# Optimization experiments

Measured on AMD Instinct MI355X. Metric: run time of the kernel, lower is better.

Reference implementation:

```python
import jax, jax.numpy as jnp
import numpy as np

HIDDEN = 1024
NUM_HEADS = 16
HEAD_DIM = HIDDEN // NUM_HEADS  # 64


def setup_inputs() -> dict:
    key = jax.random.key(0)
    ks = jax.random.split(key, 10)
    B, S = 2, 2048
    X = jax.random.normal(ks[0], (B, S, HIDDEN), dtype=jnp.float32)
    attention_mask = jnp.ones((B, 1, 1, S), dtype=jnp.int32)
    s = 1.0 / np.sqrt(HIDDEN)
    Wq = jax.random.uniform(ks[1], (HIDDEN, NUM_HEADS * HEAD_DIM), jnp.float32, -s, s)
    bq = jnp.zeros((NUM_HEADS * HEAD_DIM,), jnp.float32)
    Wk = jax.random.uniform(ks[2], (HIDDEN, HEAD_DIM), jnp.float32, -s, s)
    bk = jnp.zeros((HEAD_DIM,), jnp.float32)
    Wv = jax.random.uniform(ks[3], (HIDDEN, HEAD_DIM), jnp.float32, -s, s)
    bv = jnp.zeros((HEAD_DIM,), jnp.float32)
    Wo = jax.random.uniform(ks[4], (HIDDEN, HIDDEN), jnp.float32, -s, s)
    bo = jnp.zeros((HIDDEN,), jnp.float32)
    return {"X": X, "Wq": Wq, "bq": bq, "Wk": Wk, "bk": bk,
            "Wv": Wv, "bv": bv, "Wo": Wo, "bo": bo,
            "attention_mask": attention_mask}


def reference(X, Wq, bq, Wk, bk, Wv, bv, Wo, bo, attention_mask):
    B, S, _ = X.shape
    H, D = NUM_HEADS, HEAD_DIM
    # projections
    q = (X @ Wq + bq).reshape(B, S, H, D).transpose(0, 2, 1, 3)  # [B,H,S,D]
    k = (X @ Wk + bk)  # [B,S,D] single KV head
    v = (X @ Wv + bv)  # [B,S,D]
    # scores: broadcast single KV head across all query heads (repeat_interleave equiv)
    scores = jnp.einsum("bhsd,btd->bhst", q, k) / np.sqrt(D)  # [B,H,S,S]
    scores = jnp.where(attention_mask == 0, -jnp.inf, scores)
    weights = jax.nn.softmax(scores, axis=-1)
    # dropout in eval mode -> identity
    out = jnp.einsum("bhst,btd->bhsd", weights, v)  # [B,H,S,D]
    out = out.transpose(0, 2, 1, 3).reshape(B, S, H * D)
    return out @ Wo + bo
```

## Files before the change

### kernel.cpp

```cpp
#include <hip/hip_runtime.h>
#include <hip/hip_bf16.h>
#include <stdint.h>


#define DI __device__ __forceinline__

typedef unsigned short u16;
typedef __attribute__((ext_vector_type(8))) __bf16 bf16x8;
typedef __attribute__((ext_vector_type(4))) float f32x4;
typedef __attribute__((ext_vector_type(4))) float float4v;
typedef __attribute__((ext_vector_type(4))) u16 u16x4;

DI u16 f2bf(float f) {
  union { float f; unsigned int u; } v; v.f = f;
  unsigned int u = v.u;
  return (u16)((u + 0x7FFFu + ((u >> 16) & 1u)) >> 16);
}

DI void async16(void* lds, const void* g) {
  __builtin_amdgcn_global_load_lds(
      (const __attribute__((address_space(1))) unsigned int*)g,
      (__attribute__((address_space(3))) unsigned int*)lds, 16, 0, 0);
}

DI void stage_rows(const u16* __restrict__ g, long gstride, char* lds,
                   int nchunks, int tid) {
  int w = tid >> 6, lane = tid & 63;
  for (int base = w * 64; base < nchunks; base += 256) {
    int chunk = base + lane;
    int row = chunk >> 3;
    int cc = (chunk & 7) ^ (row & 7);
    async16(lds + base * 16, g + (long)row * gstride + cc * 8);
  }
}

DI bf16x8 read_frag(const char* lds, int row, int kchunk) {
  return *(const bf16x8*)(lds + row * 128 + ((kchunk ^ (row & 7)) << 4));
}

DI f32x4 MFMA(bf16x8 a, bf16x8 b, f32x4 c) {
  return __builtin_amdgcn_mfma_f32_16x16x32_bf16(a, b, c, 0, 0, 0);
}


__global__ void cvt_f32_bf16_kernel(const float* __restrict__ src,
                                    u16* __restrict__ dst, int n4) {
  int i = blockIdx.x * blockDim.x + threadIdx.x;
  if (i >= n4) return;
  float4v v = *(const float4v*)(src + (long)i * 4);
  u16x4 o;
  o[0] = f2bf(v[0]); o[1] = f2bf(v[1]); o[2] = f2bf(v[2]); o[3] = f2bf(v[3]);
  *(u16x4*)(dst + (long)i * 4) = o;
}

__global__ void transpose_f32_bf16(const float* __restrict__ src,
                                   u16* __restrict__ dst, int K, int N) {
  __shared__ float t[32][33];
  int nt = blockIdx.x % (N >> 5), kt = blockIdx.x / (N >> 5);
  int c = threadIdx.x & 31, r0 = threadIdx.x >> 5;
#pragma unroll
  for (int i = 0; i < 4; i++) {
    int r = r0 + i * 8;
    t[r][c] = src[(long)(kt * 32 + r) * N + nt * 32 + c];
  }
  __syncthreads();
#pragma unroll
  for (int i = 0; i < 4; i++) {
    int r = r0 + i * 8;
    dst[(long)(nt * 32 + r) * K + kt * 32 + c] = f2bf(t[c][r]);
  }
}


template <int EPI, int BN>
__global__ __launch_bounds__(256, 3) void gemm_bf16(
    const u16* __restrict__ A, const u16* __restrict__ Bt, int N, int K,
    u16* __restrict__ Qb, u16* __restrict__ Kb, u16* __restrict__ Vt,
    const float* __restrict__ bq, const float* __restrict__ bk,
    const float* __restrict__ bv, float* __restrict__ Cout,
    const float* __restrict__ bo) {
  constexpr int NF = BN / 32;
  constexpr int ACH = 1024, BCH = BN * 8;
  __shared__ __attribute__((aligned(16))) char lds[2][16384 + BN * 128];
  const int tid = threadIdx.x, lane = tid & 63, w = tid >> 6;
  const int nTiles = N / BN;
  const int mt = blockIdx.x / nTiles, nt = blockIdx.x % nTiles;
  const int m0 = mt << 7, n0 = nt * BN;
  const int wm = w >> 1, wn = w & 1;
  const int lrow = lane & 15, lk = lane >> 4;

  f32x4 acc[4][NF] = {};

  stage_rows(A + (long)m0 * K, K, lds[0], ACH, tid);
  stage_rows(Bt + (long)n0 * K, K, lds[0] + 16384, BCH, tid);
  __syncthreads();

  const int NT = K >> 6;
  int cur = 0;
  for (int t = 0; t < NT; t++) {
    if (t + 1 < NT) {
      stage_rows(A + (long)m0 * K + (t + 1) * 64, K, lds[cur ^ 1], ACH, tid);
      stage_rows(Bt + (long)n0 * K + (t + 1) * 64, K, lds[cur ^ 1] + 16384,
                 BCH, tid);
    }
    const char* La = lds[cur];
    const char* Lb = lds[cur] + 16384;
#pragma unroll
    for (int kk = 0; kk < 2; kk++) {
      bf16x8 af[4], bfr[NF];
#pragma unroll
      for (int i = 0; i < 4; i++)
        af[i] = read_frag(La, wm * 64 + i * 16 + lrow, kk * 4 + lk);
#pragma unroll
      for (int i = 0; i < NF; i++)
        bfr[i] = read_frag(Lb, wn * (BN / 2) + i * 16 + lrow, kk * 4 + lk);
#pragma unroll
      for (int mf = 0; mf < 4; mf++)
#pragma unroll
        for (int nf = 0; nf < NF; nf++)
          acc[mf][nf] = MFMA(af[mf], bfr[nf], acc[mf][nf]);
    }
    __syncthreads();
    cur ^= 1;
  }

#pragma unroll
  for (int mf = 0; mf < 4; mf++) {
#pragma unroll
    for (int nf = 0; nf < NF; nf++) {
      int col = n0 + wn * (BN / 2) + nf * 16 + lrow;
#pragma unroll
      for (int r = 0; r < 4; r++) {
        int row = m0 + wm * 64 + mf * 16 + lk * 4 + r;
        float x = acc[mf][nf][r];
        if (EPI == 0) {
          if (col < 1024) {
            Qb[(long)row * 1024 + col] = f2bf((x + bq[col]) * 0.125f);
          } else if (col < 1088) {
            int d = col - 1024;
            Kb[(long)row * 64 + d] = f2bf(x + bk[d]);
          } else {
            int d = col - 1088;
            int b = row >> 11, s = row & 2047;
            Vt[((long)(b * 64 + d)) * 2048 + s] = f2bf(x + bv[d]);
          }
        } else {
          Cout[(long)row * 1024 + col] = x + bo[col];
        }
      }
    }
  }
}

__global__ __launch_bounds__(256, 4) void attn_kernel(
    const u16* __restrict__ Qb, const u16* __restrict__ Kb,
    const u16* __restrict__ Vt, u16* __restrict__ attnb) {
  __shared__ __attribute__((aligned(16))) char ldsQP[8192];
  __shared__ __attribute__((aligned(16))) char ldsK[2][8192];
  __shared__ __attribute__((aligned(16))) char ldsV[2][8192];

  const int tid = threadIdx.x, lane = tid & 63, w = tid >> 6;
  const int lrow = lane & 15, lk = lane >> 4;
  const int qt = blockIdx.x & 31;
  const int bh = blockIdx.x >> 5;
  const int b = bh >> 4, h = bh & 15;
  const int q0 = qt << 6;

  const u16* Qg = Qb + ((long)(b * 2048 + q0)) * 1024 + h * 64;
  const u16* Kg = Kb + ((long)b * 2048) * 64;
  const u16* Vg = Vt + ((long)b * 64) * 2048;

  stage_rows(Qg, 1024, ldsQP, 512, tid);
  stage_rows(Kg, 64, ldsK[0], 512, tid);
  stage_rows(Vg, 2048, ldsV[0], 512, tid);
  __syncthreads();

  bf16x8 qa[2];
#pragma unroll
  for (int kk = 0; kk < 2; kk++)
    qa[kk] = read_frag(ldsQP, w * 16 + lrow, kk * 4 + lk);

  f32x4 acc[4] = {};
  float m_run[4], l_run[4];
#pragma unroll
  for (int r = 0; r < 4; r++) { m_run[r] = -1e30f; l_run[r] = 0.f; }

  bf16x8 vones;
#pragma unroll
  for (int i = 0; i < 8; i++) vones[i] = (__bf16)1.0f;

  int cur = 0;
  for (int t = 0; t < 32; t++) {
    if (t + 1 < 32) {
      stage_rows(Kg + (t + 1) * 64 * 64, 64, ldsK[cur ^ 1], 512, tid);
      stage_rows(Vg + (t + 1) * 64, 2048, ldsV[cur ^ 1], 512, tid);
    }
    f32x4 s[4] = {};
    __builtin_amdgcn_s_setprio(1);
#pragma unroll
    for (int kk = 0; kk < 2; kk++) {
      bf16x8 kb[4];
#pragma unroll
      for (int kf = 0; kf < 4; kf++)
        kb[kf] = read_frag(ldsK[cur], kf * 16 + lrow, kk * 4 + lk);
#pragma unroll
      for (int kf = 0; kf < 4; kf++)
        s[kf] = MFMA(qa[kk], kb[kf], s[kf]);
    }
    __builtin_amdgcn_s_setprio(0);
#pragma unroll
    for (int r = 0; r < 4; r++) {
      float mx = fmaxf(fmaxf(s[0][r], s[1][r]), fmaxf(s[2][r], s[3][r]));
#pragma unroll
      for (int msk = 1; msk < 16; msk <<= 1)
        mx = fmaxf(mx, __shfl_xor(mx, msk));
      if (mx > m_run[r] + 8.f) {
        float alpha = __expf(m_run[r] - mx);
        m_run[r] = mx;
        l_run[r] *= alpha;
#pragma unroll
        for (int df = 0; df < 4; df++) acc[df][r] *= alpha;
      }
      int q = w * 16 + lk * 4 + r;
      char* prow = ldsQP + q * 128;
      int sw = (q & 7) << 4;
#pragma unroll
      for (int kf = 0; kf < 4; kf++) {
        float p = __expf(s[kf][r] - m_run[r]);
        int col = kf * 16 + lrow;
        *(u16*)(prow + (((col >> 3) << 4) ^ sw) + (col & 7) * 2) = f2bf(p);
      }
    }
    f32x4 lsum = {};
    __builtin_amdgcn_s_setprio(1);
#pragma unroll
    for (int kk = 0; kk < 2; kk++) {
      bf16x8 pa = read_frag(ldsQP, w * 16 + lrow, kk * 4 + lk);
      bf16x8 vb[4];
#pragma unroll
      for (int df = 0; df < 4; df++)
        vb[df] = read_frag(ldsV[cur], df * 16 + lrow, kk * 4 + lk);
#pragma unroll
      for (int df = 0; df < 4; df++)
        acc[df] = MFMA(pa, vb[df], acc[df]);
      lsum = MFMA(pa, vones, lsum);
    }
    __builtin_amdgcn_s_setprio(0);
#pragma unroll
    for (int r = 0; r < 4; r++) l_run[r] += lsum[r];
    __syncthreads();
    cur ^= 1;
  }

#pragma unroll
  for (int df = 0; df < 4; df++)
#pragma unroll
    for (int r = 0; r < 4; r++) {
      int qrow = q0 + w * 16 + lk * 4 + r;
      int col = h * 64 + df * 16 + lrow;
      float o = acc[df][r] / l_run[r];
      attnb[((long)(b * 2048 + qrow)) * 1024 + col] = f2bf(o);
    }
}


extern "C" void kernel_launch(void* const* d_in, const int* in_sizes, int n_in,
                              void* d_out, int out_size, void* d_ws,
                              size_t ws_size, hipStream_t stream) {
  const float* X  = (const float*)d_in[0];
  const float* Wq = (const float*)d_in[1];
  const float* bq = (const float*)d_in[2];
  const float* Wk = (const float*)d_in[3];
  const float* bk = (const float*)d_in[4];
  const float* Wv = (const float*)d_in[5];
  const float* bv = (const float*)d_in[6];
  const float* Wo = (const float*)d_in[7];
  const float* bo = (const float*)d_in[8];
  float* out = (float*)d_out;

  char* ws = (char*)d_ws;
  u16* Xbf   = (u16*)(ws);
  u16* WqkvT = (u16*)(ws + 8388608);
  u16* WoT   = (u16*)(ws + 10747904);
  u16* Qb    = (u16*)(ws + 12845056);
  u16* Kb    = (u16*)(ws + 21233664);
  u16* Vt    = (u16*)(ws + 21757952);
  u16* attnb = (u16*)(ws + 22282240);

  cvt_f32_bf16_kernel<<<4096, 256, 0, stream>>>(X, Xbf, 1048576);
  transpose_f32_bf16<<<1024, 256, 0, stream>>>(Wq, WqkvT, 1024, 1024);
  transpose_f32_bf16<<<64, 256, 0, stream>>>(Wk, WqkvT + 1024 * 1024, 1024, 64);
  transpose_f32_bf16<<<64, 256, 0, stream>>>(Wv, WqkvT + 1088 * 1024, 1024, 64);
  transpose_f32_bf16<<<1024, 256, 0, stream>>>(Wo, WoT, 1024, 1024);

  gemm_bf16<0, 64><<<576, 256, 0, stream>>>(Xbf, WqkvT, 1152, 1024, Qb, Kb, Vt,
                                            bq, bk, bv, nullptr, nullptr);
  attn_kernel<<<1024, 256, 0, stream>>>(Qb, Kb, Vt, attnb);
  gemm_bf16<1, 64><<<512, 256, 0, stream>>>(attnb, WoT, 1024, 1024, nullptr,
                                            nullptr, nullptr, nullptr, nullptr,
                                            nullptr, out, bo);
}
```

Before: 223.6 us.

## Rewrite attention with 32x32 MFMA, register-resident P, and exp2 softmax

The attention kernel now computes transposed scores S^T = K·Q^T with 32x32x16 MFMAs, so each lane holds one query column and the row max needs only one cross-lane shuffle. The probabilities are packed into bf16 and exchanged between lane halves with shuffles, which removes the LDS round-trip for P. The query tile grows to 128 rows per block (512 blocks, occupancy hint lowered to 2), and K/V staging is folded into one double-buffered LDS array. Q is pre-scaled by log2(e)/8 so exp2f can replace __expf. The price is more registers per lane and half as many blocks.

```diff
diff --git a/kernel.cpp b/kernel.cpp
--- a/kernel.cpp
+++ b/kernel.cpp
@@ -6,15 +6,23 @@
 #define DI __device__ __forceinline__
 
 typedef unsigned short u16;
+typedef unsigned int u32;
 typedef __attribute__((ext_vector_type(8))) __bf16 bf16x8;
 typedef __attribute__((ext_vector_type(4))) float f32x4;
+typedef __attribute__((ext_vector_type(16))) float f32x16;
 typedef __attribute__((ext_vector_type(4))) float float4v;
 typedef __attribute__((ext_vector_type(4))) u16 u16x4;
+typedef __attribute__((ext_vector_type(4))) u32 u32x4;
+typedef __attribute__((ext_vector_type(2))) u32 u32x2;
 
 DI u16 f2bf(float f) {
   union { float f; unsigned int u; } v; v.f = f;
   unsigned int u = v.u;
   return (u16)((u + 0x7FFFu + ((u >> 16) & 1u)) >> 16);
+}
+
+DI u32 pk2(float lo, float hi) {
+  return (u32)f2bf(lo) | ((u32)f2bf(hi) << 16);
 }
 
 DI void async16(void* lds, const void* g) {
@@ -40,6 +48,9 @@
 
 DI f32x4 MFMA(bf16x8 a, bf16x8 b, f32x4 c) {
   return __builtin_amdgcn_mfma_f32_16x16x32_bf16(a, b, c, 0, 0, 0);
+}
+DI f32x16 MFMA32(bf16x8 a, bf16x8 b, f32x16 c) {
+  return __builtin_amdgcn_mfma_f32_32x32x16_bf16(a, b, c, 0, 0, 0);
 }
 
 
@@ -135,7 +146,7 @@
         float x = acc[mf][nf][r];
         if (EPI == 0) {
           if (col < 1024) {
-            Qb[(long)row * 1024 + col] = f2bf((x + bq[col]) * 0.125f);
+            Qb[(long)row * 1024 + col] = f2bf((x + bq[col]) * 0.18033688f);
           } else if (col < 1088) {
             int d = col - 1024;
             Kb[(long)row * 64 + d] = f2bf(x + bk[d]);
@@ -152,114 +163,122 @@
   }
 }
 
-__global__ __launch_bounds__(256, 4) void attn_kernel(
+__global__ __launch_bounds__(256, 2) void attn_kernel(
     const u16* __restrict__ Qb, const u16* __restrict__ Kb,
     const u16* __restrict__ Vt, u16* __restrict__ attnb) {
-  __shared__ __attribute__((aligned(16))) char ldsQP[8192];
-  __shared__ __attribute__((aligned(16))) char ldsK[2][8192];
-  __shared__ __attribute__((aligned(16))) char ldsV[2][8192];
+  __shared__ __attribute__((aligned(16))) char ldsKV[2][16384];
 
   const int tid = threadIdx.x, lane = tid & 63, w = tid >> 6;
-  const int lrow = lane & 15, lk = lane >> 4;
-  const int qt = blockIdx.x & 31;
-  const int bh = blockIdx.x >> 5;
+  const int cq = lane & 31, hi = lane >> 5;
+  const int qt = blockIdx.x & 15;
+  const int bh = blockIdx.x >> 4;
   const int b = bh >> 4, h = bh & 15;
-  const int q0 = qt << 6;
+  const int q0 = qt << 7;
 
   const u16* Qg = Qb + ((long)(b * 2048 + q0)) * 1024 + h * 64;
   const u16* Kg = Kb + ((long)b * 2048) * 64;
   const u16* Vg = Vt + ((long)b * 64) * 2048;
 
-  stage_rows(Qg, 1024, ldsQP, 512, tid);
-  stage_rows(Kg, 64, ldsK[0], 512, tid);
-  stage_rows(Vg, 2048, ldsV[0], 512, tid);
-  __syncthreads();
-
-  bf16x8 qa[2];
-#pragma unroll
-  for (int kk = 0; kk < 2; kk++)
-    qa[kk] = read_frag(ldsQP, w * 16 + lrow, kk * 4 + lk);
-
-  f32x4 acc[4] = {};
-  float m_run[4], l_run[4];
-#pragma unroll
-  for (int r = 0; r < 4; r++) { m_run[r] = -1e30f; l_run[r] = 0.f; }
+  stage_rows(Qg, 1024, ldsKV[0], 1024, tid);
+  __syncthreads();
+  bf16x8 qa[4];
+#pragma unroll
+  for (int dk = 0; dk < 4; dk++)
+    qa[dk] = read_frag(ldsKV[0], w * 32 + cq, dk * 2 + hi);
+  __syncthreads();
+
+  stage_rows(Kg, 64, ldsKV[0], 512, tid);
+  stage_rows(Vg, 2048, ldsKV[0] + 8192, 512, tid);
+
+  f32x16 acc[2] = {};
+  float m_run = -1e30f, l_run = 0.f;
 
   bf16x8 vones;
 #pragma unroll
   for (int i = 0; i < 8; i++) vones[i] = (__bf16)1.0f;
-
-  int cur = 0;
+  __syncthreads();
+
   for (int t = 0; t < 32; t++) {
+    const char* kbuf = ldsKV[t & 1];
+    const char* vbuf = ldsKV[t & 1] + 8192;
     if (t + 1 < 32) {
-      stage_rows(Kg + (t + 1) * 64 * 64, 64, ldsK[cur ^ 1], 512, tid);
-      stage_rows(Vg + (t + 1) * 64, 2048, ldsV[cur ^ 1], 512, tid);
-    }
-    f32x4 s[4] = {};
+      stage_rows(Kg + (t + 1) * 64 * 64, 64, ldsKV[(t + 1) & 1], 512, tid);
+      stage_rows(Vg + (t + 1) * 64, 2048, ldsKV[(t + 1) & 1] + 8192, 512, tid);
+    }
+    f32x16 s[2] = {};
     __builtin_amdgcn_s_setprio(1);
 #pragma unroll
-    for (int kk = 0; kk < 2; kk++) {
-      bf16x8 kb[4];
-#pragma unroll
-      for (int kf = 0; kf < 4; kf++)
-        kb[kf] = read_frag(ldsK[cur], kf * 16 + lrow, kk * 4 + lk);
-#pragma unroll
-      for (int kf = 0; kf < 4; kf++)
-        s[kf] = MFMA(qa[kk], kb[kf], s[kf]);
-    }
+    for (int kb = 0; kb < 2; kb++)
+#pragma unroll
+      for (int dk = 0; dk < 4; dk++) {
+        bf16x8 ka = read_frag(kbuf, kb * 32 + cq, dk * 2 + hi);
+        s[kb] = MFMA32(ka, qa[dk], s[kb]);
+      }
     __builtin_amdgcn_s_setprio(0);
-#pragma unroll
-    for (int r = 0; r < 4; r++) {
-      float mx = fmaxf(fmaxf(s[0][r], s[1][r]), fmaxf(s[2][r], s[3][r]));
-#pragma unroll
-      for (int msk = 1; msk < 16; msk <<= 1)
-        mx = fmaxf(mx, __shfl_xor(mx, msk));
-      if (mx > m_run[r] + 8.f) {
-        float alpha = __expf(m_run[r] - mx);
-        m_run[r] = mx;
-        l_run[r] *= alpha;
-#pragma unroll
-        for (int df = 0; df < 4; df++) acc[df][r] *= alpha;
+    float mx = s[0][0];
+#pragma unroll
+    for (int i = 1; i < 16; i++) mx = fmaxf(mx, s[0][i]);
+#pragma unroll
+    for (int i = 0; i < 16; i++) mx = fmaxf(mx, s[1][i]);
+    mx = fmaxf(mx, __shfl_xor(mx, 32));
+    if (mx > m_run + 8.f) {
+      float al = exp2f(m_run - mx);
+      m_run = mx;
+      l_run *= al;
+#pragma unroll
+      for (int db = 0; db < 2; db++)
+#pragma unroll
+        for (int i = 0; i < 16; i++) acc[db][i] *= al;
+    }
+#pragma unroll
+    for (int kb = 0; kb < 2; kb++)
+#pragma unroll
+      for (int i = 0; i < 16; i++) s[kb][i] = exp2f(s[kb][i] - m_run);
+    bf16x8 pa[4];
+#pragma unroll
+    for (int kb = 0; kb < 2; kb++)
+#pragma unroll
+      for (int g = 0; g < 2; g++) {
+        u32 x0 = pk2(s[kb][8 * g + 0], s[kb][8 * g + 1]);
+        u32 x1 = pk2(s[kb][8 * g + 2], s[kb][8 * g + 3]);
+        u32 y0 = pk2(s[kb][8 * g + 4], s[kb][8 * g + 5]);
+        u32 y1 = pk2(s[kb][8 * g + 6], s[kb][8 * g + 7]);
+        u32 px0 = __shfl_xor(x0, 32), px1 = __shfl_xor(x1, 32);
+        u32 py0 = __shfl_xor(y0, 32), py1 = __shfl_xor(y1, 32);
+        u32x4 wv;
+        wv[0] = hi ? py0 : x0;
+        wv[1] = hi ? py1 : x1;
+        wv[2] = hi ? y0 : px0;
+        wv[3] = hi ? y1 : px1;
+        pa[kb * 2 + g] = __builtin_bit_cast(bf16x8, wv);
       }
-      int q = w * 16 + lk * 4 + r;
-      char* prow = ldsQP + q * 128;
-      int sw = (q & 7) << 4;
-#pragma unroll
-      for (int kf = 0; kf < 4; kf++) {
-        float p = __expf(s[kf][r] - m_run[r]);
-        int col = kf * 16 + lrow;
-        *(u16*)(prow + (((col >> 3) << 4) ^ sw) + (col & 7) * 2) = f2bf(p);
+    f32x16 lsum = {};
+    __builtin_amdgcn_s_setprio(1);
+#pragma unroll
+    for (int ks = 0; ks < 4; ks++) {
+#pragma unroll
+      for (int db = 0; db < 2; db++) {
+        bf16x8 va = read_frag(vbuf, db * 32 + cq, ks * 2 + hi);
+        acc[db] = MFMA32(va, pa[ks], acc[db]);
       }
-    }
-    f32x4 lsum = {};
-    __builtin_amdgcn_s_setprio(1);
-#pragma unroll
-    for (int kk = 0; kk < 2; kk++) {
-      bf16x8 pa = read_frag(ldsQP, w * 16 + lrow, kk * 4 + lk);
-      bf16x8 vb[4];
-#pragma unroll
-      for (int df = 0; df < 4; df++)
-        vb[df] = read_frag(ldsV[cur], df * 16 + lrow, kk * 4 + lk);
-#pragma unroll
-      for (int df = 0; df < 4; df++)
-        acc[df] = MFMA(pa, vb[df], acc[df]);
-      lsum = MFMA(pa, vones, lsum);
+      lsum = MFMA32(vones, pa[ks], lsum);
     }
     __builtin_amdgcn_s_setprio(0);
-#pragma unroll
-    for (int r = 0; r < 4; r++) l_run[r] += lsum[r];
+    l_run += lsum[0];
     __syncthreads();
-    cur ^= 1;
-  }
-
-#pragma unroll
-  for (int df = 0; df < 4; df++)
-#pragma unroll
-    for (int r = 0; r < 4; r++) {
-      int qrow = q0 + w * 16 + lk * 4 + r;
-      int col = h * 64 + df * 16 + lrow;
-      float o = acc[df][r] / l_run[r];
-      attnb[((long)(b * 2048 + qrow)) * 1024 + col] = f2bf(o);
+  }
+
+  float inv = 1.f / l_run;
+  long qrow = b * 2048 + q0 + w * 32 + cq;
+#pragma unroll
+  for (int db = 0; db < 2; db++)
+#pragma unroll
+    for (int qd = 0; qd < 4; qd++) {
+      int d0 = h * 64 + db * 32 + qd * 8 + 4 * hi;
+      u32x2 pr;
+      pr[0] = pk2(acc[db][qd * 4 + 0] * inv, acc[db][qd * 4 + 1] * inv);
+      pr[1] = pk2(acc[db][qd * 4 + 2] * inv, acc[db][qd * 4 + 3] * inv);
+      *(u32x2*)(attnb + qrow * 1024 + d0) = pr;
     }
 }
 
@@ -295,7 +314,7 @@
 
   gemm_bf16<0, 64><<<576, 256, 0, stream>>>(Xbf, WqkvT, 1152, 1024, Qb, Kb, Vt,
                                             bq, bk, bv, nullptr, nullptr);
-  attn_kernel<<<1024, 256, 0, stream>>>(Qb, Kb, Vt, attnb);
+  attn_kernel<<<512, 256, 0, stream>>>(Qb, Kb, Vt, attnb);
   gemm_bf16<1, 64><<<512, 256, 0, stream>>>(attnb, WoT, 1024, 1024, nullptr,
                                             nullptr, nullptr, nullptr, nullptr,
                                             nullptr, out, bo);
```

Result: faster. 218.2 us (-2.4%).
